# Kernel tuning notes

Measured on AMD Instinct MI355X. Metric: run time of the kernel, lower is better.

Reference implementation:

```python
import jax, jax.numpy as jnp
import numpy as np

N, C, H, E = 10000, 128, 256, 320000
CUTOFF = 5.0
EPS = 1e-5


def _ln(x, g, b):
    mu = jnp.mean(x, axis=-1, keepdims=True)
    var = jnp.var(x, axis=-1, keepdims=True)
    return (x - mu) * jax.lax.rsqrt(var + EPS) * g + b


def setup_inputs() -> dict:
    key = jax.random.key(0)
    ks = jax.random.split(key, 24)

    def w(k, shape, fan_in):
        return (jax.random.normal(k, shape, dtype=jnp.float32) / np.sqrt(fan_in)).astype(jnp.float32)

    inp = {}
    inp["x"] = jax.random.normal(ks[0], (N, 3), dtype=jnp.float32)
    inp["h"] = jax.random.normal(ks[1], (N, C), dtype=jnp.float32)
    inp["edge_index"] = jax.random.randint(ks[2], (2, E), 0, N, dtype=jnp.int32)
    # edge_mlp: Linear(2C+1 -> H), SiLU, Linear(H -> H), SiLU
    inp["We1"] = w(ks[3], (2 * C + 1, H), 2 * C + 1); inp["be1"] = jnp.zeros((H,), jnp.float32)
    inp["We2"] = w(ks[4], (H, H), H);                inp["be2"] = jnp.zeros((H,), jnp.float32)
    # node_mlp: Linear(C+H -> H), SiLU, Linear(H -> C)
    inp["Wn1"] = w(ks[5], (C + H, H), C + H);        inp["bn1"] = jnp.zeros((H,), jnp.float32)
    inp["Wn2"] = w(ks[6], (H, C), H);                inp["bn2"] = jnp.zeros((C,), jnp.float32)
    # residual mlp: Linear(C -> H), SiLU, Dropout(eval), Linear(H -> C)
    inp["Wm1"] = w(ks[7], (C, H), C);                inp["bm1"] = jnp.zeros((H,), jnp.float32)
    inp["Wm2"] = w(ks[8], (H, C), H);                inp["bm2"] = jnp.zeros((C,), jnp.float32)
    # layernorms
    inp["g1"] = jnp.ones((C,), jnp.float32); inp["beta1"] = jnp.zeros((C,), jnp.float32)
    inp["g2"] = jnp.ones((C,), jnp.float32); inp["beta2"] = jnp.zeros((C,), jnp.float32)
    return inp


def reference(x, h, edge_index, We1, be1, We2, be2, Wn1, bn1, Wn2, bn2,
              Wm1, bm1, Wm2, bm2, g1, beta1, g2, beta2):
    row, col = edge_index[0], edge_index[1]

    h_res = h
    hn = _ln(h, g1, beta1)                              # [N, C]

    # ---- EGNN layer ----
    rel = x[row] - x[col]                               # [E, 3]
    dist = jnp.linalg.norm(rel, axis=-1, keepdims=True) # [E, 1]
    edge_in = jnp.concatenate([hn[row], hn[col], dist], axis=-1)  # [E, 2C+1]
    m = jax.nn.silu(edge_in @ We1 + be1)
    m = jax.nn.silu(m @ We2 + be2)                      # [E, H]

    d = dist[:, 0]
    Ccut = 0.5 * (jnp.cos(d * jnp.pi / CUTOFF) + 1.0)
    Ccut = Ccut * (d <= CUTOFF) * (d >= 0.0)
    m = m * Ccut[:, None]

    # mean-aggregate messages at target nodes (edge_index[1])
    sums = jax.ops.segment_sum(m, col, num_segments=N)          # [N, H]
    cnt = jax.ops.segment_sum(jnp.ones((m.shape[0],), m.dtype), col, num_segments=N)
    m_aggr = sums / jnp.maximum(cnt, 1.0)[:, None]

    hd = jax.nn.silu(jnp.concatenate([hn, m_aggr], axis=-1) @ Wn1 + bn1) @ Wn2 + bn2
    h_egnn = hn + hd

    h1 = h_res + h_egnn

    # ---- norm2 + MLP residual (dropout = identity in eval) ----
    h2 = _ln(h1, g2, beta2)
    h2 = jax.nn.silu(h2 @ Wm1 + bm1) @ Wm2 + bm2
    return h1 + h2
```

## Files before the change

### kernel.cpp

```cpp
#include <hip/hip_runtime.h>

#define NN 10000
#define CC 128
#define HH 256
#define EE 320000
#define ETILE 96
#define EBLOCKS 3334

typedef __bf16 bf16_t;
typedef __bf16 bf16x8 __attribute__((ext_vector_type(8)));
typedef __bf16 bf16x4 __attribute__((ext_vector_type(4)));
typedef float f32x4 __attribute__((ext_vector_type(4)));

__device__ __forceinline__ float silu_f(float v) {
#if __has_builtin(__builtin_amdgcn_rcpf)
  return v * __builtin_amdgcn_rcpf(1.0f + __expf(-v));
#else
  return v / (1.0f + __expf(-v));
#endif
}

template<int RE, int KD, int SA, int NT>
__device__ __forceinline__ void gemm_lg(const bf16_t* sAa, const bf16_t* __restrict__ BT,
                                        int nwavebase, int lr, int quad, f32x4 acc[RE][NT]) {
  for (int kk = 0; kk < KD; kk += 32) {
    bf16x8 a[RE]; bf16x8 b[NT];
#pragma unroll
    for (int re = 0; re < RE; re++)
      a[re] = *(const bf16x8*)(sAa + (re * 16 + lr) * SA + kk + quad * 8);
#pragma unroll
    for (int ce = 0; ce < NT; ce++)
      b[ce] = *(const bf16x8*)(BT + (size_t)(nwavebase + ce * 16 + lr) * KD + kk + quad * 8);
#pragma unroll
    for (int re = 0; re < RE; re++)
#pragma unroll
      for (int ce = 0; ce < NT; ce++)
        acc[re][ce] = __builtin_amdgcn_mfma_f32_16x16x32_bf16(a[re], b[ce], acc[re][ce], 0, 0, 0);
  }
}

__global__ __launch_bounds__(256) void prep_kernel(
    const float* __restrict__ We1, const float* __restrict__ We2,
    const float* __restrict__ Wn1, const float* __restrict__ Wn2,
    const float* __restrict__ Wm1, const float* __restrict__ Wm2,
    bf16_t* __restrict__ We1T, bf16_t* __restrict__ We2T,
    bf16_t* __restrict__ Wn1T, bf16_t* __restrict__ Wn2T,
    bf16_t* __restrict__ Wm1T, bf16_t* __restrict__ Wm2T,
    float* __restrict__ sums, int* __restrict__ cnt, uint4* __restrict__ edat) {
  int i = blockIdx.x * 256 + threadIdx.x;
  if (i < 327680) {
    const float* src; bf16_t* dst; int K, Nc, idx;
    if      (i < 65536)  { src = We1; dst = We1T; K = 256; Nc = 256; idx = i; }
    else if (i < 131072) { src = We2; dst = We2T; K = 256; Nc = 256; idx = i - 65536; }
    else if (i < 229376) { src = Wn1; dst = Wn1T; K = 384; Nc = 256; idx = i - 131072; }
    else if (i < 262144) { src = Wn2; dst = Wn2T; K = 256; Nc = 128; idx = i - 229376; }
    else if (i < 294912) { src = Wm1; dst = Wm1T; K = 128; Nc = 256; idx = i - 262144; }
    else                 { src = Wm2; dst = Wm2T; K = 256; Nc = 128; idx = i - 294912; }
    int n = idx / K, k = idx - n * K;
    dst[idx] = (bf16_t)src[(size_t)k * Nc + n];
  } else if (i < 327680 + 640000) {
    f32x4 z = {0.f, 0.f, 0.f, 0.f};
    ((f32x4*)sums)[i - 327680] = z;
  } else if (i < 327680 + 640000 + 2500) {
    int4 z = {0, 0, 0, 0};
    ((int4*)cnt)[i - 967680] = z;
  } else if (i < 327680 + 640000 + 2500 + 64) {
    uint4 z = {0u, 0u, 0u, 0u};
    edat[EE + (i - 970180)] = z;
  }
}

__global__ __launch_bounds__(256, 4) void node_pre_kernel(
    const float* __restrict__ h, const float* __restrict__ g1,
    const float* __restrict__ bt1,
    const bf16_t* __restrict__ We1T, const float* __restrict__ be1,
    bf16_t* __restrict__ hn16, bf16_t* __restrict__ PQ) {
  __shared__ __align__(16) bf16_t sHn[16 * 136];
  int tid = threadIdx.x;
  int lane = tid & 63, wave = tid >> 6;
  int lr = lane & 15, quad = lane >> 4;
  int n0 = blockIdx.x * 16;

  {
    int node = tid >> 4, c0 = (tid & 15) * 8;
    size_t base = (size_t)(n0 + node) * CC;
    f32x4 u0 = *(const f32x4*)(h + base + c0);
    f32x4 u1 = *(const f32x4*)(h + base + c0 + 4);
    float s = 0.f, sq = 0.f;
#pragma unroll
    for (int j = 0; j < 4; j++) { s += u0[j] + u1[j]; sq += u0[j] * u0[j] + u1[j] * u1[j]; }
#pragma unroll
    for (int o = 8; o > 0; o >>= 1) { s += __shfl_xor(s, o); sq += __shfl_xor(sq, o); }
    float mu = s * (1.0f / CC);
    float var = sq * (1.0f / CC) - mu * mu;
    float rs = rsqrtf(var + 1e-5f);
    f32x4 gg0 = *(const f32x4*)(g1 + c0), gg1 = *(const f32x4*)(g1 + c0 + 4);
    f32x4 bb0 = *(const f32x4*)(bt1 + c0), bb1 = *(const f32x4*)(bt1 + c0 + 4);
    bf16x8 ov;
#pragma unroll
    for (int j = 0; j < 4; j++) {
      ov[j] = (bf16_t)((u0[j] - mu) * rs * gg0[j] + bb0[j]);
      ov[j + 4] = (bf16_t)((u1[j] - mu) * rs * gg1[j] + bb1[j]);
    }
    *(bf16x8*)(sHn + node * 136 + c0) = ov;
    *(bf16x8*)(hn16 + base + c0) = ov;
  }
  __syncthreads();

  bool isQ = wave >= 2;
  int rbase = (wave & 1) * 128;
  int koff = isQ ? 128 : 0;
  f32x4 zf = {0.f, 0.f, 0.f, 0.f};
  f32x4 acc[8];
#pragma unroll
  for (int i = 0; i < 8; i++) acc[i] = zf;
  for (int kk = 0; kk < 128; kk += 32) {
    bf16x8 b = *(const bf16x8*)(sHn + lr * 136 + kk + quad * 8);
    bf16x8 a[8];
#pragma unroll
    for (int re = 0; re < 8; re++)
      a[re] = *(const bf16x8*)(We1T + (size_t)(rbase + re * 16 + lr) * 256 + koff + kk + quad * 8);
#pragma unroll
    for (int re = 0; re < 8; re++)
      acc[re] = __builtin_amdgcn_mfma_f32_16x16x32_bf16(a[re], b, acc[re], 0, 0, 0);
  }
#pragma unroll
  for (int re = 0; re < 8; re++) {
    int cb = rbase + re * 16 + quad * 4;
    f32x4 bb = isQ ? zf : *(const f32x4*)(be1 + cb);
    bf16x4 o;
#pragma unroll
    for (int r = 0; r < 4; r++) o[r] = (bf16_t)(acc[re][r] + bb[r]);
    *(bf16x4*)(PQ + (size_t)(n0 + lr) * 512 + (isQ ? 256 : 0) + cb) = o;
  }
}

__global__ __launch_bounds__(256) void count_kernel(const int* __restrict__ ei, int* __restrict__ cnt) {
  int e = blockIdx.x * 256 + threadIdx.x;
  atomicAdd(&cnt[ei[EE + e]], 1);
}

__global__ __launch_bounds__(1024) void scan_kernel(const int* __restrict__ cnt, int* __restrict__ cursor) {
  __shared__ int wsum[16];
  int tid = threadIdx.x, wave = tid >> 6, lane = tid & 63;
  int base = tid * 10;
  int v[10]; int S = 0;
#pragma unroll
  for (int j = 0; j < 10; j++) {
    int i = base + j;
    v[j] = (i < NN) ? cnt[i] : 0;
    S += v[j];
  }
  int s = S;
#pragma unroll
  for (int off = 1; off < 64; off <<= 1) { int t = __shfl_up(s, off); if (lane >= off) s += t; }
  if (lane == 63) wsum[wave] = s;
  __syncthreads();
  if (tid < 16) {
    int ws = wsum[tid];
#pragma unroll
    for (int off = 1; off < 16; off <<= 1) { int t = __shfl_up(ws, off); if (tid >= off) ws += t; }
    wsum[tid] = ws;
  }
  __syncthreads();
  int ex = ((wave > 0) ? wsum[wave - 1] : 0) + s - S;
#pragma unroll
  for (int j = 0; j < 10; j++) {
    int i = base + j;
    if (i < NN) cursor[i] = ex;
    ex += v[j];
  }
}

__global__ __launch_bounds__(256) void scatter_kernel(const int* __restrict__ ei,
                                                      const float* __restrict__ x,
                                                      int* __restrict__ cursor,
                                                      uint4* __restrict__ edat) {
  int e = blockIdx.x * 256 + threadIdx.x;
  int r = ei[e], c = ei[EE + e];
  float dx = x[3 * r] - x[3 * c];
  float dy = x[3 * r + 1] - x[3 * c + 1];
  float dz = x[3 * r + 2] - x[3 * c + 2];
  float d = sqrtf(dx * dx + dy * dy + dz * dz);
  float cc = (d <= 5.0f) ? 0.5f * (cosf(d * 0.6283185307179586f) + 1.0f) : 0.0f;
  int pos = atomicAdd(&cursor[c], 1);
  uint4 v = {(unsigned)r, (unsigned)c, __float_as_uint(d), __float_as_uint(cc)};
  edat[pos] = v;
}

__global__ __launch_bounds__(512, 4) void edge_mlp_kernel(
    const uint4* __restrict__ edat, const bf16_t* __restrict__ PQ,
    const float* __restrict__ We1last,
    const bf16_t* __restrict__ We2T, const float* __restrict__ be2,
    float* __restrict__ sums) {
  __shared__ __align__(16) bf16_t sM1[ETILE * 264];
  __shared__ int sRow[ETILE], sCol[ETILE];
  __shared__ float sD[ETILE], sCc[ETILE];
  __shared__ unsigned long long sMaskA;
  __shared__ unsigned sMaskB;
  int tid = threadIdx.x;
  int lane = tid & 63, wave = tid >> 6;
  int lr = lane & 15, quad = lane >> 4;
  int e0 = blockIdx.x * ETILE;

  if (tid < ETILE) {
    uint4 v = edat[e0 + tid];
    sRow[tid] = (int)v.x; sCol[tid] = (int)v.y;
    sD[tid] = __uint_as_float(v.z); sCc[tid] = __uint_as_float(v.w);
  }
  __syncthreads();

  if (tid < ETILE) {
    int fl = (tid > 0) && (sCol[tid] != sCol[tid - 1]);
    unsigned long long m = __ballot(fl);
    if (tid == 0) sMaskA = m;
    if (tid == 64) sMaskB = (unsigned)m;
  }

#pragma unroll 3
  for (int i = 0; i < 6; i++) {
    int o = tid + i * 512;
    int e = o >> 5, q = o & 31;
    int k0 = q * 8;
    int row = sRow[e], col = sCol[e];
    float d = sD[e];
    bf16x8 pv = *(const bf16x8*)(PQ + (size_t)row * 512 + k0);
    bf16x8 qv = *(const bf16x8*)(PQ + (size_t)col * 512 + 256 + k0);
    f32x4 wl0 = *(const f32x4*)(We1last + k0);
    f32x4 wl1 = *(const f32x4*)(We1last + k0 + 4);
    bf16x8 m;
#pragma unroll
    for (int j = 0; j < 4; j++) {
      m[j] = (bf16_t)silu_f((float)pv[j] + (float)qv[j] + d * wl0[j]);
      m[j + 4] = (bf16_t)silu_f((float)pv[j + 4] + (float)qv[j + 4] + d * wl1[j]);
    }
    *(bf16x8*)(sM1 + e * 264 + k0) = m;
  }
  __syncthreads();

  f32x4 zf = {0.f, 0.f, 0.f, 0.f};
  f32x4 acc[6][2];
#pragma unroll
  for (int i = 0; i < 6; i++) { acc[i][0] = zf; acc[i][1] = zf; }
  for (int kk = 0; kk < 256; kk += 32) {
    bf16x8 a[6]; bf16x8 b[2];
#pragma unroll
    for (int re = 0; re < 6; re++)
      a[re] = *(const bf16x8*)(sM1 + (re * 16 + lr) * 264 + kk + quad * 8);
#pragma unroll
    for (int ce = 0; ce < 2; ce++)
      b[ce] = *(const bf16x8*)(We2T + (size_t)(wave * 32 + ce * 16 + lr) * 256 + kk + quad * 8);
#pragma unroll
    for (int re = 0; re < 6; re++)
#pragma unroll
      for (int ce = 0; ce < 2; ce++)
        acc[re][ce] = __builtin_amdgcn_mfma_f32_16x16x32_bf16(a[re], b[ce], acc[re][ce], 0, 0, 0);
  }

  float be2v[2];
#pragma unroll
  for (int ce = 0; ce < 2; ce++) be2v[ce] = be2[wave * 32 + ce * 16 + lr];
#pragma unroll
  for (int re = 0; re < 6; re++) {
    f32x4 cc = *(const f32x4*)(sCc + re * 16 + quad * 4);
#pragma unroll
    for (int ce = 0; ce < 2; ce++)
#pragma unroll
      for (int r = 0; r < 4; r++)
        acc[re][ce][r] = silu_f(acc[re][ce][r] + be2v[ce]) * cc[r];
  }

  {
    unsigned long long mA = sMaskA;
    unsigned long long mB = (unsigned long long)sMaskB;
    int lo = 0;
    while (lo < ETILE) {
      int hi;
      if (lo < 63) {
        unsigned long long t = mA & (~0ull << (lo + 1));
        hi = t ? (__ffsll((long long)t) - 1)
               : (mB ? 64 + __ffsll((long long)mB) - 1 : ETILE);
      } else {
        unsigned long long t1 = mB & (~0ull << (lo - 63));
        hi = t1 ? 64 + __ffsll((long long)t1) - 1 : ETILE;
      }
      float tv0 = 0.f, tv1 = 0.f;
#pragma unroll
      for (int re = 0; re < 6; re++) {
        int t0 = re * 16, t1e = t0 + 16;
        if (t1e <= lo || t0 >= hi) continue;
        if (t0 >= lo && t1e <= hi) {
#pragma unroll
          for (int r = 0; r < 4; r++) { tv0 += acc[re][0][r]; tv1 += acc[re][1][r]; }
        } else {
          int eb = t0 + quad * 4;
#pragma unroll
          for (int r = 0; r < 4; r++) {
            int e = eb + r;
            bool in = (e >= lo) && (e < hi);
            tv0 += in ? acc[re][0][r] : 0.0f;
            tv1 += in ? acc[re][1][r] : 0.0f;
          }
        }
      }
      tv0 += __shfl_xor(tv0, 16); tv0 += __shfl_xor(tv0, 32);
      tv1 += __shfl_xor(tv1, 16); tv1 += __shfl_xor(tv1, 32);
      if (quad == 0) {
        int colv = sCol[lo];
        atomicAdd(&sums[(size_t)colv * HH + wave * 32 + lr], tv0);
        atomicAdd(&sums[(size_t)colv * HH + wave * 32 + 16 + lr], tv1);
      }
      lo = hi;
    }
  }
}

__global__ __launch_bounds__(256, 2) void node_fused_kernel(
    const float* __restrict__ h, const bf16_t* __restrict__ hn16,
    const float* __restrict__ sums, const int* __restrict__ cnt,
    const bf16_t* __restrict__ Wn1T, const float* __restrict__ bn1,
    const bf16_t* __restrict__ Wn2T, const float* __restrict__ bn2,
    const float* __restrict__ g2, const float* __restrict__ bt2,
    const bf16_t* __restrict__ Wm1T, const float* __restrict__ bm1,
    const bf16_t* __restrict__ Wm2T, const float* __restrict__ bm2,
    float* __restrict__ out) {
  __shared__ __align__(16) bf16_t sA1[32 * 392];
  __shared__ __align__(16) bf16_t sM[32 * 264];
  __shared__ __align__(16) float sH1[32 * 132];
  __shared__ __align__(16) bf16_t sLn[32 * 136];
  __shared__ float sRc[32];
  int tid = threadIdx.x;
  int lane = tid & 63, wave = tid >> 6;
  int lr = lane & 15, quad = lane >> 4;
  int n0 = blockIdx.x * 32;

  if (tid < 32) {
    int node = n0 + tid;
    sRc[tid] = (node < NN) ? 1.0f / fmaxf((float)cnt[node], 1.0f) : 0.0f;
  }
  __syncthreads();

#pragma unroll
  for (int i = 0; i < 6; i++) {
    int o = tid + i * 256;
    int e = o / 48, q = o - e * 48;
    int node = n0 + e;
    if (q < 16) {
      uint4 v = {0u, 0u, 0u, 0u};
      if (node < NN) v = *(const uint4*)(hn16 + (size_t)node * CC + q * 8);
      *(uint4*)(sA1 + e * 392 + q * 8) = v;
    } else {
      bf16x8 bv = {};
      if (node < NN) {
        float rc = sRc[e];
        const float* sp = sums + (size_t)node * HH + (q - 16) * 8;
#pragma unroll
        for (int k2 = 0; k2 < 8; k2++) bv[k2] = (bf16_t)(sp[k2] * rc);
      }
      *(bf16x8*)(sA1 + e * 392 + 128 + (q - 16) * 8) = bv;
    }
  }
  __syncthreads();

  f32x4 zf = {0.f, 0.f, 0.f, 0.f};
  {
    f32x4 acc[2][4];
#pragma unroll
    for (int i = 0; i < 2; i++)
#pragma unroll
      for (int j = 0; j < 4; j++) acc[i][j] = zf;
    gemm_lg<2, 384, 392, 4>(sA1, Wn1T, wave * 64, lr, quad, acc);
#pragma unroll
    for (int ce = 0; ce < 4; ce++) {
      int n = wave * 64 + ce * 16 + lr;
      float b1 = bn1[n];
#pragma unroll
      for (int re = 0; re < 2; re++)
#pragma unroll
        for (int r = 0; r < 4; r++)
          sM[(re * 16 + quad * 4 + r) * 264 + n] = (bf16_t)silu_f(acc[re][ce][r] + b1);
    }
  }
  __syncthreads();

  {
    f32x4 acc[2][2];
#pragma unroll
    for (int i = 0; i < 2; i++) { acc[i][0] = zf; acc[i][1] = zf; }
    gemm_lg<2, 256, 264, 2>(sM, Wn2T, wave * 32, lr, quad, acc);
#pragma unroll
    for (int ce = 0; ce < 2; ce++) {
      int n = wave * 32 + ce * 16 + lr;
      float b2 = bn2[n];
#pragma unroll
      for (int re = 0; re < 2; re++)
#pragma unroll
        for (int r = 0; r < 4; r++) {
          int node = re * 16 + quad * 4 + r;
          float hv = 0.f;
          if (n0 + node < NN) hv = h[(size_t)(n0 + node) * CC + n];
          sH1[node * 132 + n] = hv + (float)sA1[node * 392 + n] + acc[re][ce][r] + b2;
        }
    }
  }
  __syncthreads();

  {
    int node = tid >> 3, c0 = (tid & 7) * 16;
    f32x4 u[4];
    float s = 0.f, sq = 0.f;
#pragma unroll
    for (int j = 0; j < 4; j++) {
      u[j] = *(const f32x4*)(sH1 + node * 132 + c0 + j * 4);
#pragma unroll
      for (int r = 0; r < 4; r++) { s += u[j][r]; sq += u[j][r] * u[j][r]; }
    }
    s += __shfl_xor(s, 1); sq += __shfl_xor(sq, 1);
    s += __shfl_xor(s, 2); sq += __shfl_xor(sq, 2);
    s += __shfl_xor(s, 4); sq += __shfl_xor(sq, 4);
    float mu = s * (1.0f / CC);
    float var = sq * (1.0f / CC) - mu * mu;
    float rs = rsqrtf(var + 1e-5f);
#pragma unroll
    for (int j2 = 0; j2 < 2; j2++) {
      f32x4 gg0 = *(const f32x4*)(g2 + c0 + j2 * 8);
      f32x4 gg1 = *(const f32x4*)(g2 + c0 + j2 * 8 + 4);
      f32x4 bb0 = *(const f32x4*)(bt2 + c0 + j2 * 8);
      f32x4 bb1 = *(const f32x4*)(bt2 + c0 + j2 * 8 + 4);
      bf16x8 ov;
#pragma unroll
      for (int r = 0; r < 4; r++) {
        ov[r] = (bf16_t)((u[j2 * 2][r] - mu) * rs * gg0[r] + bb0[r]);
        ov[r + 4] = (bf16_t)((u[j2 * 2 + 1][r] - mu) * rs * gg1[r] + bb1[r]);
      }
      *(bf16x8*)(sLn + node * 136 + c0 + j2 * 8) = ov;
    }
  }
  __syncthreads();

  {
    f32x4 acc[2][4];
#pragma unroll
    for (int i = 0; i < 2; i++)
#pragma unroll
      for (int j = 0; j < 4; j++) acc[i][j] = zf;
    gemm_lg<2, 128, 136, 4>(sLn, Wm1T, wave * 64, lr, quad, acc);
#pragma unroll
    for (int ce = 0; ce < 4; ce++) {
      int n = wave * 64 + ce * 16 + lr;
      float b1 = bm1[n];
#pragma unroll
      for (int re = 0; re < 2; re++)
#pragma unroll
        for (int r = 0; r < 4; r++)
          sM[(re * 16 + quad * 4 + r) * 264 + n] = (bf16_t)silu_f(acc[re][ce][r] + b1);
    }
  }
  __syncthreads();

  {
    f32x4 acc[2][2];
#pragma unroll
    for (int i = 0; i < 2; i++) { acc[i][0] = zf; acc[i][1] = zf; }
    gemm_lg<2, 256, 264, 2>(sM, Wm2T, wave * 32, lr, quad, acc);
#pragma unroll
    for (int ce = 0; ce < 2; ce++) {
      int n = wave * 32 + ce * 16 + lr;
      float b2 = bm2[n];
#pragma unroll
      for (int re = 0; re < 2; re++)
#pragma unroll
        for (int r = 0; r < 4; r++) {
          int node = re * 16 + quad * 4 + r;
          if (n0 + node < NN)
            out[(size_t)(n0 + node) * CC + n] = sH1[node * 132 + n] + acc[re][ce][r] + b2;
        }
    }
  }
}

extern "C" void kernel_launch(void* const* d_in, const int* in_sizes, int n_in,
                              void* d_out, int out_size, void* d_ws, size_t ws_size,
                              hipStream_t stream) {
  const float* x    = (const float*)d_in[0];
  const float* h    = (const float*)d_in[1];
  const int*   ei   = (const int*)d_in[2];
  const float* We1  = (const float*)d_in[3];
  const float* be1  = (const float*)d_in[4];
  const float* We2  = (const float*)d_in[5];
  const float* be2  = (const float*)d_in[6];
  const float* Wn1  = (const float*)d_in[7];
  const float* bn1  = (const float*)d_in[8];
  const float* Wn2  = (const float*)d_in[9];
  const float* bn2  = (const float*)d_in[10];
  const float* Wm1  = (const float*)d_in[11];
  const float* bm1  = (const float*)d_in[12];
  const float* Wm2  = (const float*)d_in[13];
  const float* bm2  = (const float*)d_in[14];
  const float* g1   = (const float*)d_in[15];
  const float* bt1  = (const float*)d_in[16];
  const float* g2   = (const float*)d_in[17];
  const float* bt2  = (const float*)d_in[18];
  float* out = (float*)d_out;

  char* wp = (char*)d_ws;
  size_t off = 0;
  auto alloc = [&](size_t bytes) -> void* {
    void* p = wp + off;
    off = (off + bytes + 255) & ~(size_t)255;
    return p;
  };

  bf16_t* hn16   = (bf16_t*)alloc((size_t)NN * CC * 2);
  bf16_t* PQ     = (bf16_t*)alloc((size_t)NN * 512 * 2);
  float*  sums   = (float*)alloc((size_t)NN * HH * 4);
  int*    cnt    = (int*)alloc((size_t)NN * 4);
  int*    cursor = (int*)alloc((size_t)NN * 4);
  uint4*  edat   = (uint4*)alloc((size_t)(EBLOCKS * ETILE) * 16);
  bf16_t* We1T   = (bf16_t*)alloc(256 * 256 * 2);
  bf16_t* We2T   = (bf16_t*)alloc(256 * 256 * 2);
  bf16_t* Wn1T   = (bf16_t*)alloc(256 * 384 * 2);
  bf16_t* Wn2T   = (bf16_t*)alloc(128 * 256 * 2);
  bf16_t* Wm1T   = (bf16_t*)alloc(256 * 128 * 2);
  bf16_t* Wm2T   = (bf16_t*)alloc(128 * 256 * 2);

  prep_kernel<<<3791, 256, 0, stream>>>(We1, We2, Wn1, Wn2, Wm1, Wm2,
                                        We1T, We2T, Wn1T, Wn2T, Wm1T, Wm2T,
                                        sums, cnt, edat);

  node_pre_kernel<<<NN / 16, 256, 0, stream>>>(h, g1, bt1, We1T, be1, hn16, PQ);

  count_kernel<<<EE / 256, 256, 0, stream>>>(ei, cnt);
  scan_kernel<<<1, 1024, 0, stream>>>(cnt, cursor);
  scatter_kernel<<<EE / 256, 256, 0, stream>>>(ei, x, cursor, edat);

  edge_mlp_kernel<<<EBLOCKS, 512, 0, stream>>>(edat, PQ, We1 + 256 * 256,
                                               We2T, be2, sums);

  node_fused_kernel<<<(NN + 31) / 32, 256, 0, stream>>>(h, hn16, sums, cnt,
                                                        Wn1T, bn1, Wn2T, bn2,
                                                        g2, bt2, Wm1T, bm1, Wm2T, bm2, out);
}
```

Measured before the change: 296.9 us.

## Fold edge counting into node_pre and split edge MLP staging into two K halves

The separate count kernel is removed: node_pre_kernel (625 blocks × 256 threads) now performs the per-target atomic counts, two edges per thread, which saves a launch. In edge_mlp_kernel, the first-layer activation staging is split into two 128-wide K halves held in separate LDS buffers. The second half is staged while the first half's MFMA GEMM runs, so gather and SiLU work overlaps with matrix math. The LDS footprint is about the same, but an extra barrier is added and the counting atomics now contend inside the node_pre kernel.

```diff
diff --git a/kernel.cpp b/kernel.cpp
--- a/kernel.cpp
+++ b/kernel.cpp
@@ -74,12 +74,19 @@
     const float* __restrict__ h, const float* __restrict__ g1,
     const float* __restrict__ bt1,
     const bf16_t* __restrict__ We1T, const float* __restrict__ be1,
+    const int* __restrict__ ei, int* __restrict__ cnt,
     bf16_t* __restrict__ hn16, bf16_t* __restrict__ PQ) {
   __shared__ __align__(16) bf16_t sHn[16 * 136];
   int tid = threadIdx.x;
   int lane = tid & 63, wave = tid >> 6;
   int lr = lane & 15, quad = lane >> 4;
   int n0 = blockIdx.x * 16;
+
+  {
+    int t = blockIdx.x * 256 + tid;
+    atomicAdd(&cnt[ei[EE + t]], 1);
+    atomicAdd(&cnt[ei[EE + t + 160000]], 1);
+  }
 
   {
     int node = tid >> 4, c0 = (tid & 15) * 8;
@@ -133,11 +140,6 @@
     for (int r = 0; r < 4; r++) o[r] = (bf16_t)(acc[re][r] + bb[r]);
     *(bf16x4*)(PQ + (size_t)(n0 + lr) * 512 + (isQ ? 256 : 0) + cb) = o;
   }
-}
-
-__global__ __launch_bounds__(256) void count_kernel(const int* __restrict__ ei, int* __restrict__ cnt) {
-  int e = blockIdx.x * 256 + threadIdx.x;
-  atomicAdd(&cnt[ei[EE + e]], 1);
 }
 
 __global__ __launch_bounds__(1024) void scan_kernel(const int* __restrict__ cnt, int* __restrict__ cursor) {
@@ -193,7 +195,7 @@
     const float* __restrict__ We1last,
     const bf16_t* __restrict__ We2T, const float* __restrict__ be2,
     float* __restrict__ sums) {
-  __shared__ __align__(16) bf16_t sM1[ETILE * 264];
+  __shared__ __align__(16) bf16_t sM1[2][ETILE * 136];
   __shared__ int sRow[ETILE], sCol[ETILE];
   __shared__ float sD[ETILE], sCc[ETILE];
   __shared__ unsigned long long sMaskA;
@@ -217,45 +219,58 @@
     if (tid == 64) sMaskB = (unsigned)m;
   }
 
-#pragma unroll 3
-  for (int i = 0; i < 6; i++) {
-    int o = tid + i * 512;
-    int e = o >> 5, q = o & 31;
-    int k0 = q * 8;
-    int row = sRow[e], col = sCol[e];
-    float d = sD[e];
-    bf16x8 pv = *(const bf16x8*)(PQ + (size_t)row * 512 + k0);
-    bf16x8 qv = *(const bf16x8*)(PQ + (size_t)col * 512 + 256 + k0);
-    f32x4 wl0 = *(const f32x4*)(We1last + k0);
-    f32x4 wl1 = *(const f32x4*)(We1last + k0 + 4);
-    bf16x8 m;
-#pragma unroll
-    for (int j = 0; j < 4; j++) {
-      m[j] = (bf16_t)silu_f((float)pv[j] + (float)qv[j] + d * wl0[j]);
-      m[j + 4] = (bf16_t)silu_f((float)pv[j + 4] + (float)qv[j + 4] + d * wl1[j]);
-    }
-    *(bf16x8*)(sM1 + e * 264 + k0) = m;
-  }
-  __syncthreads();
+  auto stage = [&](int hf) {
+#pragma unroll
+    for (int i = 0; i < 3; i++) {
+      int o = tid + i * 512;
+      int e = o >> 4, q = o & 15;
+      int k0 = q * 8;
+      int row = sRow[e], col = sCol[e];
+      float d = sD[e];
+      bf16x8 pv = *(const bf16x8*)(PQ + (size_t)row * 512 + hf * 128 + k0);
+      bf16x8 qv = *(const bf16x8*)(PQ + (size_t)col * 512 + 256 + hf * 128 + k0);
+      f32x4 wl0 = *(const f32x4*)(We1last + hf * 128 + k0);
+      f32x4 wl1 = *(const f32x4*)(We1last + hf * 128 + k0 + 4);
+      bf16x8 m;
+#pragma unroll
+      for (int j = 0; j < 4; j++) {
+        m[j] = (bf16_t)silu_f((float)pv[j] + (float)qv[j] + d * wl0[j]);
+        m[j + 4] = (bf16_t)silu_f((float)pv[j + 4] + (float)qv[j + 4] + d * wl1[j]);
+      }
+      *(bf16x8*)(&sM1[hf][0] + e * 136 + k0) = m;
+    }
+  };
 
   f32x4 zf = {0.f, 0.f, 0.f, 0.f};
   f32x4 acc[6][2];
+
+  auto gemm_half = [&](int hf) {
+    for (int kk = 0; kk < 128; kk += 32) {
+      bf16x8 a[6]; bf16x8 b[2];
+#pragma unroll
+      for (int re = 0; re < 6; re++)
+        a[re] = *(const bf16x8*)(&sM1[hf][0] + (re * 16 + lr) * 136 + kk + quad * 8);
+#pragma unroll
+      for (int ce = 0; ce < 2; ce++)
+        b[ce] = *(const bf16x8*)(We2T + (size_t)(wave * 32 + ce * 16 + lr) * 256 + hf * 128 + kk + quad * 8);
+#pragma unroll
+      for (int re = 0; re < 6; re++)
+#pragma unroll
+        for (int ce = 0; ce < 2; ce++)
+          acc[re][ce] = __builtin_amdgcn_mfma_f32_16x16x32_bf16(a[re], b[ce], acc[re][ce], 0, 0, 0);
+    }
+  };
+
+  stage(0);
+  __syncthreads();
+
 #pragma unroll
   for (int i = 0; i < 6; i++) { acc[i][0] = zf; acc[i][1] = zf; }
-  for (int kk = 0; kk < 256; kk += 32) {
-    bf16x8 a[6]; bf16x8 b[2];
-#pragma unroll
-    for (int re = 0; re < 6; re++)
-      a[re] = *(const bf16x8*)(sM1 + (re * 16 + lr) * 264 + kk + quad * 8);
-#pragma unroll
-    for (int ce = 0; ce < 2; ce++)
-      b[ce] = *(const bf16x8*)(We2T + (size_t)(wave * 32 + ce * 16 + lr) * 256 + kk + quad * 8);
-#pragma unroll
-    for (int re = 0; re < 6; re++)
-#pragma unroll
-      for (int ce = 0; ce < 2; ce++)
-        acc[re][ce] = __builtin_amdgcn_mfma_f32_16x16x32_bf16(a[re], b[ce], acc[re][ce], 0, 0, 0);
-  }
+
+  stage(1);
+  gemm_half(0);
+  __syncthreads();
+  gemm_half(1);
 
   float be2v[2];
 #pragma unroll
@@ -528,9 +543,9 @@
                                         We1T, We2T, Wn1T, Wn2T, Wm1T, Wm2T,
                                         sums, cnt, edat);
 
-  node_pre_kernel<<<NN / 16, 256, 0, stream>>>(h, g1, bt1, We1T, be1, hn16, PQ);
-
-  count_kernel<<<EE / 256, 256, 0, stream>>>(ei, cnt);
+  node_pre_kernel<<<NN / 16, 256, 0, stream>>>(h, g1, bt1, We1T, be1,
+                                               ei, cnt, hn16, PQ);
+
   scan_kernel<<<1, 1024, 0, stream>>>(cnt, cursor);
   scatter_kernel<<<EE / 256, 256, 0, stream>>>(ei, x, cursor, edat);
 
```

Measured after the change: 297.6 us. Within noise of the previous version (+0.2%).
